# Performance work log

Measured on AMD Instinct MI355X. Metric: run time of the kernel, lower is better.

Reference implementation:

```python
import jax, jax.numpy as jnp
import numpy as np

B, V, D, NH, DH = 1, 6, 256, 8, 32
L, ZP = 4, 4
BEV = 80
Q = BEV * BEV
SHAPES = [(56, 100), (28, 50), (14, 25), (7, 13)]
N = sum(h * w for h, w in SHAPES)
PAD_H, PAD_W = 448, 800
PC = (-48.0, -48.0, -5.0, 48.0, 48.0, 3.0)
EPS = 1e-5


def _ref3d():
    # get_reference_points + pc_range scaling; the original overwrites the z channel
    # with scaled-x (code bug: ref_3d[...,2:3] = ref_3d[...,:1]*zrange+zmin) -> reproduced faithfully,
    # so all ZP pillar points are identical.
    u = jnp.arange(Q)
    xs = ((u % BEV).astype(jnp.float32) + 0.5) / BEV
    ys = ((u // BEV).astype(jnp.float32) + 0.5) / BEV
    x = xs * (PC[3] - PC[0]) + PC[0]
    y = ys * (PC[4] - PC[1]) + PC[1]
    z = x * (PC[5] - PC[2]) + PC[2]
    p = jnp.stack([x, y, z], -1)  # [Q,3]
    return jnp.broadcast_to(p[None], (ZP, Q, 3))


def _project(l2i):
    # l2i: [B,V,4,4] -> normalized coords [B,V,Q,ZP,2], validity mask [B,V,Q,ZP]
    pts = _ref3d().reshape(-1, 3)
    pts_h = jnp.concatenate([pts, jnp.ones_like(pts[:, :1])], -1)  # [ZP*Q,4]
    ip = jnp.einsum('bvij,nj->bvni', l2i, pts_h)                   # [B,V,ZP*Q,4]
    zc = ip[..., 2]
    xy = ip[..., :2] / jnp.clip(zc, EPS, None)[..., None]
    xn = xy[..., 0] / PAD_W
    yn = xy[..., 1] / PAD_H
    m = (zc > EPS) & (xn > 0) & (xn < 1) & (yn > 0) & (yn < 1)
    coords = jnp.stack([xn, yn], -1).reshape(B, V, ZP, Q, 2).transpose(0, 1, 3, 2, 4)
    mask = m.reshape(B, V, ZP, Q).transpose(0, 1, 3, 2)
    return coords, mask


def _forward(feat0, feat1, feat2, feat3, lidar2img_mat, bev_emb, level_embeds,
             view_embeds, value_W, value_b, off_W, off_b, aw_W, aw_b, out_W, out_b):
    feats = [feat0, feat1, feat2, feat3]
    parts = []
    for l, f in enumerate(feats):
        h, w = SHAPES[l]
        x = f.reshape(B, V, D, h * w).transpose(0, 1, 3, 2)  # [B,V,hw,D]
        x = x + view_embeds[None, :, None, :] + level_embeds[l]
        parts.append(x)
    feat_flat = jnp.concatenate(parts, axis=2)  # [B,V,N,D]

    coords, mask = _project(lidar2img_mat)
    mask_any = mask.any(-1)                                            # [B,V,Q]
    count = jnp.clip(mask_any.sum(1).astype(jnp.float32), 1.0, None)   # [B,Q]

    value = (feat_flat.reshape(B * V, N, D) @ value_W + value_b).reshape(B * V, N, NH, DH)
    off = (bev_emb @ off_W + off_b).reshape(Q, NH, L, ZP, 2)
    aw = jax.nn.softmax((bev_emb @ aw_W + aw_b).reshape(Q, NH, L * ZP), -1).reshape(Q, NH, L, ZP)
    ref = coords.reshape(B * V, Q, ZP, 2)

    out = jnp.zeros((B * V, Q, NH, DH), feat_flat.dtype)
    start = 0
    for l, (h, w) in enumerate(SHAPES):
        v_l = value[:, start:start + h * w].transpose(0, 2, 1, 3).reshape(B * V * NH, h * w, DH)
        start += h * w
        loc = ref[:, :, None, :, :] + off[None, :, :, l] / jnp.array([w, h], feat_flat.dtype)
        loc = loc.transpose(0, 2, 1, 3, 4).reshape(B * V * NH, Q * ZP, 2)
        # grid_sample(align_corners=False, padding='zeros') with grid 2*loc-1
        gx = loc[..., 0] * w - 0.5
        gy = loc[..., 1] * h - 0.5
        x0 = jnp.floor(gx).astype(jnp.int32)
        y0 = jnp.floor(gy).astype(jnp.int32)
        wx1 = gx - x0
        wy1 = gy - y0

        def corner(xi, yi, wt):
            valid = (xi >= 0) & (xi < w) & (yi >= 0) & (yi < h)
            lin = jnp.clip(yi, 0, h - 1) * w + jnp.clip(xi, 0, w - 1)
            g = jnp.take_along_axis(v_l, lin[..., None], axis=1)
            return g * (wt * valid)[..., None]

        s = (corner(x0, y0, (1 - wx1) * (1 - wy1)) + corner(x0 + 1, y0, wx1 * (1 - wy1))
             + corner(x0, y0 + 1, (1 - wx1) * wy1) + corner(x0 + 1, y0 + 1, wx1 * wy1))
        s = s.reshape(B * V, NH, Q, ZP, DH)
        out = out + jnp.einsum('vhqzd,qhz->vqhd', s, aw[:, :, l])

    attn = out.reshape(B, V, Q, D)
    slots = (attn * mask_any[..., None]).sum(1) / count[..., None]
    slots = slots @ out_W + out_b
    return bev_emb[None] + slots  # dropout is identity at inference


def setup_inputs() -> dict:
    key = jax.random.key(0)
    ks = jax.random.split(key, 16)
    s = 0.02
    return {
        'feat0': jax.random.normal(ks[0], (B, V, D) + SHAPES[0], jnp.float32),
        'feat1': jax.random.normal(ks[1], (B, V, D) + SHAPES[1], jnp.float32),
        'feat2': jax.random.normal(ks[2], (B, V, D) + SHAPES[2], jnp.float32),
        'feat3': jax.random.normal(ks[3], (B, V, D) + SHAPES[3], jnp.float32),
        'lidar2img_mat': jax.random.normal(ks[4], (B, V, 4, 4), jnp.float32) * 50.0,
        'bev_emb': jax.random.normal(ks[5], (Q, D), jnp.float32) * s,
        'level_embeds': jax.random.normal(ks[6], (L, D), jnp.float32) * s,
        'view_embeds': jax.random.normal(ks[7], (V, D), jnp.float32) * s,
        'value_W': jax.random.normal(ks[8], (D, D), jnp.float32) * s,
        'value_b': jnp.zeros((D,), jnp.float32),
        'off_W': jax.random.normal(ks[9], (D, NH * L * ZP * 2), jnp.float32) * s,
        'off_b': jnp.zeros((NH * L * ZP * 2,), jnp.float32),
        'aw_W': jax.random.normal(ks[10], (D, NH * L * ZP), jnp.float32) * s,
        'aw_b': jnp.zeros((NH * L * ZP,), jnp.float32),
        'out_W': jax.random.normal(ks[11], (D, D), jnp.float32) * s,
        'out_b': jnp.zeros((D,), jnp.float32),
    }


def reference(feat0, feat1, feat2, feat3, lidar2img_mat, bev_emb, level_embeds,
              view_embeds, value_W, value_b, off_W, off_b, aw_W, aw_b, out_W, out_b):
    return _forward(feat0, feat1, feat2, feat3, lidar2img_mat, bev_emb, level_embeds,
                    view_embeds, value_W, value_b, off_W, off_b, aw_W, aw_b, out_W, out_b)
```

## Files before the change

### kernel.cpp

```cpp
#include <hip/hip_runtime.h>
#include <cstdint>
#include <cstddef>

#define NV 6
#define ND 256
#define NHEAD 8
#define NBEV 80
#define NQ 6400
#define NTOK 7441
#define MROWS (NV * NTOK)
#define FEPS 1e-5f

#define VROWT 698
#define VBLKS (VROWT * 2)
#define OABLKS 300
#define GBLKS (VBLKS + OABLKS)
#define GCHUNK (GBLKS / 8)

typedef __attribute__((ext_vector_type(8))) short bfx8;
typedef __attribute__((ext_vector_type(4))) float fx4;
typedef __attribute__((ext_vector_type(4))) _Float16 hx4;
typedef __attribute__((ext_vector_type(4))) unsigned short usx4;

__device__ __forceinline__ unsigned short f2bf(float x) {
    uint32_t u = __builtin_bit_cast(uint32_t, x);
    u += 0x7FFFu + ((u >> 16) & 1u);
    return (unsigned short)(u >> 16);
}
__device__ __forceinline__ float lof(uint32_t u) {
    return __builtin_bit_cast(float, u << 16);
}
__device__ __forceinline__ float hif(uint32_t u) {
    return __builtin_bit_cast(float, u & 0xFFFF0000u);
}

__global__ __launch_bounds__(256) void k_prep(
        const float* __restrict__ l2i, const float* __restrict__ ve,
        const float* __restrict__ le, const float* __restrict__ vW,
        const float* __restrict__ vB, const float* __restrict__ oW,
        const float* __restrict__ aW, const float* __restrict__ outW,
        float2* __restrict__ coords, int* __restrict__ mask,
        unsigned short* __restrict__ vWt, unsigned short* __restrict__ oaWt,
        unsigned short* __restrict__ outWt, float* __restrict__ emb_proj) {
    int bid = blockIdx.x;
    int t = threadIdx.x;
    if (bid < 150) {
        int idx = bid * 256 + t;
        int v = idx / NQ, q = idx - v * NQ;
        float xs = ((float)(q % NBEV) + 0.5f) / (float)NBEV;
        float ys = ((float)(q / NBEV) + 0.5f) / (float)NBEV;
        float x = xs * 96.0f - 48.0f;
        float y = ys * 96.0f - 48.0f;
        float z = x * 8.0f - 5.0f;
        const float* M = l2i + v * 16;
        float ip0 = M[0] * x + M[1] * y + M[2] * z + M[3];
        float ip1 = M[4] * x + M[5] * y + M[6] * z + M[7];
        float ip2 = M[8] * x + M[9] * y + M[10] * z + M[11];
        float dz = fmaxf(ip2, FEPS);
        float xn = ip0 / dz / 800.0f;
        float yn = ip1 / dz / 448.0f;
        bool m = (ip2 > FEPS) && (xn > 0.0f) && (xn < 1.0f) && (yn > 0.0f) && (yn < 1.0f);
        coords[idx] = make_float2(xn, yn);
        mask[idx] = m ? 1 : 0;
    } else if (bid < 406) {
        int e = (bid - 150) * 256 + t;
        int k = e >> 8, n = e & 255;
        vWt[(size_t)n * 256 + k] = f2bf(vW[(size_t)k * 256 + n]);
    } else if (bid < 662) {
        int e = (bid - 406) * 256 + t;
        int k = e >> 8, n = e & 255;
        oaWt[(size_t)n * 256 + k] = f2bf(oW[(size_t)k * 256 + n]);
    } else if (bid < 790) {
        int e = (bid - 662) * 256 + t;
        int k = e >> 7, n = e & 127;
        oaWt[(size_t)(256 + n) * 256 + k] = f2bf(aW[(size_t)k * 128 + n]);
    } else if (bid < 1046) {
        int e = (bid - 790) * 256 + t;
        int k = e >> 8, n = e & 255;
        outWt[(size_t)n * 256 + k] = f2bf(outW[(size_t)k * 256 + n]);
    } else {
        int blk = bid - 1046;
        int v = blk >> 2, l = blk & 3;
        float acc = vB[t];
        for (int d = 0; d < ND; ++d)
            acc += (ve[v * ND + d] + le[l * ND + d]) * vW[d * ND + t];
        emb_proj[blk * ND + t] = acc;
    }
}

__global__ __launch_bounds__(256) void k_gemms(
        const float* __restrict__ f0, const float* __restrict__ f1,
        const float* __restrict__ f2, const float* __restrict__ f3,
        const unsigned short* __restrict__ vWt, const float* __restrict__ emb_proj,
        unsigned short* __restrict__ value,
        const float* __restrict__ bev, const unsigned short* __restrict__ oaWt,
        const float* __restrict__ oB, const float* __restrict__ aB,
        float* __restrict__ off, float* __restrict__ aw_pre) {
    __shared__ unsigned short As[64][40];
    __shared__ unsigned short Bs[128][40];
    __shared__ const float* rowptr[64];
    __shared__ int rowstride[64];
    __shared__ int rowemb[64];
    int b = blockIdx.x;
    int lb = (b & 7) * GCHUNK + (b >> 3);
    int t = threadIdx.x;
    int lane = t & 63, w = t >> 6;
    int wm = w >> 1, wn = w & 1;
    int lr = lane & 15, lk = lane >> 4;
    int mA = t & 63, kg = t >> 6;

    fx4 acc[2][4];
#pragma unroll
    for (int i = 0; i < 2; ++i)
#pragma unroll
        for (int j = 0; j < 4; ++j) acc[i][j] = (fx4)0.0f;

    if (lb < VBLKS) {
        int m0 = (lb >> 1) * 64, c0 = (lb & 1) * 128;
        if (t < 64) {
            int m = m0 + t;
            if (m >= MROWS) m = MROWS - 1;
            int v = m / NTOK, n = m - v * NTOK;
            int l, p, hw;
            const float* base;
            if (n < 5600)      { l = 0; p = n;        hw = 5600; base = f0; }
            else if (n < 7000) { l = 1; p = n - 5600; hw = 1400; base = f1; }
            else if (n < 7350) { l = 2; p = n - 7000; hw = 350;  base = f2; }
            else               { l = 3; p = n - 7350; hw = 91;   base = f3; }
            rowptr[t] = base + (size_t)v * ND * hw + p;
            rowstride[t] = hw;
            rowemb[t] = v * 4 + l;
        }
        __syncthreads();
        const unsigned short* bp = vWt + (size_t)(c0 + (t >> 1)) * 256 + (t & 1) * 16;
        const float* rp = rowptr[mA];
        int rs = rowstride[mA];
        for (int k0 = 0; k0 < 256; k0 += 32) {
            float va[8];
#pragma unroll
            for (int i = 0; i < 8; ++i)
                va[i] = rp[(size_t)(k0 + kg * 8 + i) * rs];
            bfx8 a8;
#pragma unroll
            for (int i = 0; i < 8; ++i) a8[i] = (short)f2bf(va[i]);
            *(bfx8*)&As[mA][kg * 8] = a8;
            *(bfx8*)&Bs[t >> 1][(t & 1) * 16] = *(const bfx8*)(bp + k0);
            *(bfx8*)&Bs[t >> 1][(t & 1) * 16 + 8] = *(const bfx8*)(bp + k0 + 8);
            __syncthreads();
            bfx8 af[2], bf[4];
#pragma unroll
            for (int f = 0; f < 2; ++f)
                af[f] = *(bfx8*)&As[wm * 32 + f * 16 + lr][lk * 8];
#pragma unroll
            for (int f = 0; f < 4; ++f)
                bf[f] = *(bfx8*)&Bs[wn * 64 + f * 16 + lr][lk * 8];
#pragma unroll
            for (int fm = 0; fm < 2; ++fm)
#pragma unroll
                for (int fn = 0; fn < 4; ++fn)
                    acc[fm][fn] = __builtin_amdgcn_mfma_f32_16x16x32_bf16(
                        af[fm], bf[fn], acc[fm][fn], 0, 0, 0);
            __syncthreads();
        }
#pragma unroll
        for (int fm = 0; fm < 2; ++fm) {
#pragma unroll
            for (int fn = 0; fn < 4; ++fn) {
                int col = c0 + wn * 64 + fn * 16 + lr;
#pragma unroll
                for (int r = 0; r < 4; ++r) {
                    int rl = wm * 32 + fm * 16 + lk * 4 + r;
                    int m = m0 + rl;
                    if (m < MROWS) {
                        float e = emb_proj[(size_t)rowemb[rl] * ND + col];
                        value[(size_t)m * ND + col] = f2bf(acc[fm][fn][r] + e);
                    }
                }
            }
        }
    } else {
        int r6 = lb - VBLKS;
        int m0 = (r6 / 3) * 64, c0 = (r6 % 3) * 128;
        const float* ap = bev + (size_t)(m0 + mA) * 256 + kg * 8;
        const unsigned short* bp = oaWt + (size_t)(c0 + (t >> 1)) * 256 + (t & 1) * 16;
        for (int k0 = 0; k0 < 256; k0 += 32) {
            float va[8];
            *(float4*)&va[0] = *(const float4*)(ap + k0);
            *(float4*)&va[4] = *(const float4*)(ap + k0 + 4);
            bfx8 a8;
#pragma unroll
            for (int i = 0; i < 8; ++i) a8[i] = (short)f2bf(va[i]);
            *(bfx8*)&As[mA][kg * 8] = a8;
            *(bfx8*)&Bs[t >> 1][(t & 1) * 16] = *(const bfx8*)(bp + k0);
            *(bfx8*)&Bs[t >> 1][(t & 1) * 16 + 8] = *(const bfx8*)(bp + k0 + 8);
            __syncthreads();
            bfx8 af[2], bf[4];
#pragma unroll
            for (int f = 0; f < 2; ++f)
                af[f] = *(bfx8*)&As[wm * 32 + f * 16 + lr][lk * 8];
#pragma unroll
            for (int f = 0; f < 4; ++f)
                bf[f] = *(bfx8*)&Bs[wn * 64 + f * 16 + lr][lk * 8];
#pragma unroll
            for (int fm = 0; fm < 2; ++fm)
#pragma unroll
                for (int fn = 0; fn < 4; ++fn)
                    acc[fm][fn] = __builtin_amdgcn_mfma_f32_16x16x32_bf16(
                        af[fm], bf[fn], acc[fm][fn], 0, 0, 0);
            __syncthreads();
        }
        if (c0 < 256) {
#pragma unroll
            for (int fm = 0; fm < 2; ++fm) {
#pragma unroll
                for (int fn = 0; fn < 4; ++fn) {
                    int col = c0 + wn * 64 + fn * 16 + lr;
                    float bs = oB[col];
#pragma unroll
                    for (int r = 0; r < 4; ++r) {
                        int m = m0 + wm * 32 + fm * 16 + lk * 4 + r;
                        off[(size_t)m * 256 + col] = acc[fm][fn][r] + bs;
                    }
                }
            }
        } else {
#pragma unroll
            for (int fm = 0; fm < 2; ++fm) {
#pragma unroll
                for (int fn = 0; fn < 4; ++fn) {
                    int col = wn * 64 + fn * 16 + lr;
                    float bs = aB[col];
#pragma unroll
                    for (int r = 0; r < 4; ++r) {
                        int m = m0 + wm * 32 + fm * 16 + lk * 4 + r;
                        aw_pre[(size_t)m * 128 + col] = acc[fm][fn][r] + bs;
                    }
                }
            }
        }
    }
}

#define SQB 2
__global__ __launch_bounds__(256) void k_sample(
        const float2* __restrict__ coords, const int* __restrict__ mask,
        const float* __restrict__ off, const float* __restrict__ awlog,
        const unsigned short* __restrict__ value, float* __restrict__ slots) {
    __shared__ float aw_s[SQB][128];
    __shared__ unsigned short lin_s[SQB][NV][128][4];
    __shared__ _Float16 w_s[SQB][NV][128][4];
    __shared__ float2 cxy_s[SQB][NV];
    __shared__ int msk_s[SQB][NV];

    int b = blockIdx.x;
    int lb = (b & 7) * (NQ / SQB / 8) + (b >> 3);
    int q0 = lb * SQB;
    int t = threadIdx.x;
    if (t < SQB * NV) {
        int qq = t / NV, v = t - qq * NV;
        msk_s[qq][v] = mask[v * NQ + q0 + qq];
        cxy_s[qq][v] = coords[v * NQ + q0 + qq];
    }
    {
        int qq = t >> 7, c2 = t & 127;
        aw_s[qq][c2] = awlog[(size_t)(q0 + qq) * 128 + c2];
    }
    __syncthreads();
    if (t < SQB * NHEAD) {
        int qq = t >> 3, h = t & 7;
        float* p = &aw_s[qq][h * 16];
        float mx = p[0];
#pragma unroll
        for (int i = 1; i < 16; ++i) mx = fmaxf(mx, p[i]);
        float e[16];
        float s = 0.0f;
#pragma unroll
        for (int i = 0; i < 16; ++i) { e[i] = __expf(p[i] - mx); s += e[i]; }
        float inv = 1.0f / s;
#pragma unroll
        for (int i = 0; i < 16; ++i) p[i] = e[i] * inv;
    }
    __syncthreads();

    const int LW[4] = {100, 50, 25, 13};
    const int LH[4] = {56, 28, 14, 7};
    const int LST[4] = {0, 5600, 7000, 7350};
    for (int idx = t; idx < SQB * NV * 128; idx += 256) {
        int c2 = idx & 127;
        int rem = idx >> 7;
        int qq = rem / NV, v = rem - qq * NV;
        if (!msk_s[qq][v]) continue;
        int ll = (c2 >> 2) & 3;
        int iwl = LW[ll], ihl = LH[ll], st = LST[ll];
        float wl = (float)iwl, hl = (float)ihl;
        float2 o2 = *(const float2*)&off[(size_t)(q0 + qq) * 256 + 2 * c2];
        float2 cc = cxy_s[qq][v];
        float gx = cc.x * wl + o2.x - 0.5f;
        float gy = cc.y * hl + o2.y - 0.5f;
        float fxf = floorf(gx), fyf = floorf(gy);
        int x0 = (int)fxf, y0 = (int)fyf;
        float wx = gx - fxf, wy = gy - fyf;
        bool bx0 = (unsigned)x0 < (unsigned)iwl;
        bool bx1 = (unsigned)(x0 + 1) < (unsigned)iwl;
        bool by0 = (unsigned)y0 < (unsigned)ihl;
        bool by1 = (unsigned)(y0 + 1) < (unsigned)ihl;
        int cx0 = min(max(x0, 0), iwl - 1);
        int cx1 = min(max(x0 + 1, 0), iwl - 1);
        int cy0 = min(max(y0, 0), ihl - 1);
        int cy1 = min(max(y0 + 1, 0), ihl - 1);
        float wa = aw_s[qq][c2];
        int r0 = st + cy0 * iwl, r1 = st + cy1 * iwl;
        usx4 lin;
        lin.x = (unsigned short)(r0 + cx0);
        lin.y = (unsigned short)(r0 + cx1);
        lin.z = (unsigned short)(r1 + cx0);
        lin.w = (unsigned short)(r1 + cx1);
        hx4 ww;
        ww.x = (_Float16)((bx0 && by0) ? (1.0f - wx) * (1.0f - wy) * wa : 0.0f);
        ww.y = (_Float16)((bx1 && by0) ? wx * (1.0f - wy) * wa : 0.0f);
        ww.z = (_Float16)((bx0 && by1) ? (1.0f - wx) * wy * wa : 0.0f);
        ww.w = (_Float16)((bx1 && by1) ? wx * wy * wa : 0.0f);
        *(usx4*)lin_s[qq][v][c2] = lin;
        *(hx4*)w_s[qq][v][c2] = ww;
    }
    __syncthreads();

    int qq = t >> 7, cp = t & 127;
    int hb = (cp >> 4) * 16;
    float acc0 = 0.0f, acc1 = 0.0f;
    int cnt = 0;
#pragma unroll
    for (int v = 0; v < NV; ++v) cnt += msk_s[qq][v];
    for (int v = 0; v < NV; ++v) {
        if (!msk_s[qq][v]) continue;
        const uint32_t* vb = (const uint32_t*)(value + (size_t)v * NTOK * 256) + cp;
#pragma unroll
        for (int ci = 0; ci < 16; ++ci) {
            int c2 = hb + ci;
            usx4 lin = *(const usx4*)lin_s[qq][v][c2];
            hx4 wh = *(const hx4*)w_s[qq][v][c2];
            uint32_t u0 = vb[(size_t)lin.x * 128];
            uint32_t u1 = vb[(size_t)lin.y * 128];
            uint32_t u2 = vb[(size_t)lin.z * 128];
            uint32_t u3 = vb[(size_t)lin.w * 128];
            float w0 = (float)wh.x, w1 = (float)wh.y;
            float w2 = (float)wh.z, w3 = (float)wh.w;
            acc0 += w0 * lof(u0) + w1 * lof(u1) + w2 * lof(u2) + w3 * lof(u3);
            acc1 += w0 * hif(u0) + w1 * hif(u1) + w2 * hif(u2) + w3 * hif(u3);
        }
    }
    float invc = 1.0f / fmaxf((float)cnt, 1.0f);
    *(float2*)&slots[(size_t)(q0 + qq) * 256 + 2 * cp] = make_float2(acc0 * invc, acc1 * invc);
}

__global__ __launch_bounds__(256) void k_out(
        const float* __restrict__ A, const unsigned short* __restrict__ Bt,
        const float* __restrict__ bias, const float* __restrict__ addsrc,
        float* __restrict__ out) {
    __shared__ unsigned short As[64][40];
    __shared__ unsigned short Bs[128][40];
    int t = threadIdx.x;
    int m0 = blockIdx.x * 64, c0 = blockIdx.y * 128;
    int lane = t & 63, w = t >> 6;
    int wm = w >> 1, wn = w & 1;
    int lr = lane & 15, lk = lane >> 4;
    int mA = t & 63, kg = t >> 6;
    const float* ap = A + (size_t)(m0 + mA) * 256 + kg * 8;
    const unsigned short* bp = Bt + (size_t)(c0 + (t >> 1)) * 256 + (t & 1) * 16;
    fx4 acc[2][4];
#pragma unroll
    for (int i = 0; i < 2; ++i)
#pragma unroll
        for (int j = 0; j < 4; ++j) acc[i][j] = (fx4)0.0f;
    for (int k0 = 0; k0 < 256; k0 += 32) {
        float va[8];
        *(float4*)&va[0] = *(const float4*)(ap + k0);
        *(float4*)&va[4] = *(const float4*)(ap + k0 + 4);
        bfx8 a8;
#pragma unroll
        for (int i = 0; i < 8; ++i) a8[i] = (short)f2bf(va[i]);
        *(bfx8*)&As[mA][kg * 8] = a8;
        *(bfx8*)&Bs[t >> 1][(t & 1) * 16] = *(const bfx8*)(bp + k0);
        *(bfx8*)&Bs[t >> 1][(t & 1) * 16 + 8] = *(const bfx8*)(bp + k0 + 8);
        __syncthreads();
        bfx8 af[2], bf[4];
#pragma unroll
        for (int f = 0; f < 2; ++f)
            af[f] = *(bfx8*)&As[wm * 32 + f * 16 + lr][lk * 8];
#pragma unroll
        for (int f = 0; f < 4; ++f)
            bf[f] = *(bfx8*)&Bs[wn * 64 + f * 16 + lr][lk * 8];
#pragma unroll
        for (int fm = 0; fm < 2; ++fm)
#pragma unroll
            for (int fn = 0; fn < 4; ++fn)
                acc[fm][fn] = __builtin_amdgcn_mfma_f32_16x16x32_bf16(
                    af[fm], bf[fn], acc[fm][fn], 0, 0, 0);
        __syncthreads();
    }
#pragma unroll
    for (int fm = 0; fm < 2; ++fm) {
#pragma unroll
        for (int fn = 0; fn < 4; ++fn) {
            int col = c0 + wn * 64 + fn * 16 + lr;
            float bs = bias[col];
#pragma unroll
            for (int r = 0; r < 4; ++r) {
                int m = m0 + wm * 32 + fm * 16 + lk * 4 + r;
                out[(size_t)m * 256 + col] =
                    acc[fm][fn][r] + bs + addsrc[(size_t)m * 256 + col];
            }
        }
    }
}

extern "C" void kernel_launch(void* const* d_in, const int* in_sizes, int n_in,
                              void* d_out, int out_size, void* d_ws, size_t ws_size,
                              hipStream_t stream) {
    const float* f0   = (const float*)d_in[0];
    const float* f1   = (const float*)d_in[1];
    const float* f2   = (const float*)d_in[2];
    const float* f3   = (const float*)d_in[3];
    const float* l2i  = (const float*)d_in[4];
    const float* bev  = (const float*)d_in[5];
    const float* le   = (const float*)d_in[6];
    const float* ve   = (const float*)d_in[7];
    const float* vW   = (const float*)d_in[8];
    const float* vB   = (const float*)d_in[9];
    const float* oW   = (const float*)d_in[10];
    const float* oB   = (const float*)d_in[11];
    const float* aW   = (const float*)d_in[12];
    const float* aB   = (const float*)d_in[13];
    const float* outW = (const float*)d_in[14];
    const float* outB = (const float*)d_in[15];
    float* out = (float*)d_out;

    char* ws = (char*)d_ws;
    size_t o = 0;
    auto alloc = [&](size_t bytes) {
        void* p = ws + o;
        o += (bytes + 255) & ~(size_t)255;
        return p;
    };
    float2* coords   = (float2*)alloc((size_t)NV * NQ * sizeof(float2));
    int*    mask     = (int*)alloc((size_t)NV * NQ * sizeof(int));
    float*  emb_proj = (float*)alloc((size_t)24 * ND * sizeof(float));
    float*  off      = (float*)alloc((size_t)NQ * 256 * sizeof(float));
    float*  aw_pre   = (float*)alloc((size_t)NQ * 128 * sizeof(float));
    float*  slots    = (float*)alloc((size_t)NQ * 256 * sizeof(float));
    unsigned short* value = (unsigned short*)alloc((size_t)MROWS * ND * sizeof(short));
    unsigned short* vWt   = (unsigned short*)alloc((size_t)256 * 256 * sizeof(short));
    unsigned short* oaWt  = (unsigned short*)alloc((size_t)384 * 256 * sizeof(short));
    unsigned short* outWt = (unsigned short*)alloc((size_t)256 * 256 * sizeof(short));

    k_prep<<<1070, 256, 0, stream>>>(l2i, ve, le, vW, vB, oW, aW, outW,
                                     coords, mask, vWt, oaWt, outWt, emb_proj);
    k_gemms<<<GBLKS, 256, 0, stream>>>(f0, f1, f2, f3, vWt, emb_proj, value,
                                       bev, oaWt, oB, aB, off, aw_pre);
    k_sample<<<NQ / SQB, 256, 0, stream>>>(coords, mask, off, aw_pre, value, slots);
    dim3 gout(NQ / 64, 2);
    k_out<<<gout, 256, 0, stream>>>(slots, outWt, outB, bev, out);
}
```

Before: 204.6 us.

## Pre-transpose features to bf16 row-major and enlarge GEMM tiles to 128x128

The prep kernel now transposes the channel-major feature maps into a token-major bf16 buffer through a shared-memory tile, and converts the BEV embedding to bf16. The GEMM kernel can then load A with contiguous vector reads instead of strided fp32 gathers. It also moves to 128x128 tiles with a 64-wide K step, giving more MFMA work per block. The cost is an extra round trip of the transposed data through global memory and fewer, larger GEMM blocks.

```diff
diff --git a/kernel.cpp b/kernel.cpp
--- a/kernel.cpp
+++ b/kernel.cpp
@@ -9,13 +9,24 @@
 #define NQ 6400
 #define NTOK 7441
 #define MROWS (NV * NTOK)
+#define MROWSP 44672
 #define FEPS 1e-5f
 
-#define VROWT 698
-#define VBLKS (VROWT * 2)
-#define OABLKS 300
-#define GBLKS (VBLKS + OABLKS)
+#define VBLKS 698
+#define GBLKS 848
 #define GCHUNK (GBLKS / 8)
+
+#define PR_PROJ 150
+#define PR_TR   2832
+#define PR_BEV  800
+#define PB0 PR_PROJ
+#define PB1 (PB0 + PR_TR)
+#define PB2 (PB1 + PR_BEV)
+#define PB3 (PB2 + 256)
+#define PB4 (PB3 + 256)
+#define PB5 (PB4 + 128)
+#define PB6 (PB5 + 256)
+#define PBT (PB6 + 24)
 
 typedef __attribute__((ext_vector_type(8))) short bfx8;
 typedef __attribute__((ext_vector_type(4))) float fx4;
@@ -35,16 +46,20 @@
 }
 
 __global__ __launch_bounds__(256) void k_prep(
-        const float* __restrict__ l2i, const float* __restrict__ ve,
-        const float* __restrict__ le, const float* __restrict__ vW,
-        const float* __restrict__ vB, const float* __restrict__ oW,
-        const float* __restrict__ aW, const float* __restrict__ outW,
+        const float* __restrict__ f0, const float* __restrict__ f1,
+        const float* __restrict__ f2, const float* __restrict__ f3,
+        const float* __restrict__ l2i, const float* __restrict__ bev,
+        const float* __restrict__ ve, const float* __restrict__ le,
+        const float* __restrict__ vW, const float* __restrict__ vB,
+        const float* __restrict__ oW, const float* __restrict__ aW,
+        const float* __restrict__ outW,
         float2* __restrict__ coords, int* __restrict__ mask,
+        unsigned short* __restrict__ featT, unsigned short* __restrict__ bevh,
         unsigned short* __restrict__ vWt, unsigned short* __restrict__ oaWt,
         unsigned short* __restrict__ outWt, float* __restrict__ emb_proj) {
     int bid = blockIdx.x;
     int t = threadIdx.x;
-    if (bid < 150) {
+    if (bid < PB0) {
         int idx = bid * 256 + t;
         int v = idx / NQ, q = idx - v * NQ;
         float xs = ((float)(q % NBEV) + 0.5f) / (float)NBEV;
@@ -62,24 +77,63 @@
         bool m = (ip2 > FEPS) && (xn > 0.0f) && (xn < 1.0f) && (yn > 0.0f) && (yn < 1.0f);
         coords[idx] = make_float2(xn, yn);
         mask[idx] = m ? 1 : 0;
-    } else if (bid < 406) {
-        int e = (bid - 150) * 256 + t;
+    } else if (bid < PB1) {
+        __shared__ float T[64][65];
+        int idx = bid - PB0;
+        int v = idx / 472;
+        int rem = idx - v * 472;
+        int mt = rem >> 2, kt = rem & 3;
+        int hw, p0, st;
+        const float* base;
+        if (mt < 88)       { base = f0; hw = 5600; st = 0;    p0 = mt * 64; }
+        else if (mt < 110) { base = f1; hw = 1400; st = 5600; p0 = (mt - 88) * 64; }
+        else if (mt < 116) { base = f2; hw = 350;  st = 7000; p0 = (mt - 110) * 64; }
+        else               { base = f3; hw = 91;   st = 7350; p0 = (mt - 116) * 64; }
+        int k0 = kt * 64;
+        const float* src = base + (size_t)v * 256 * hw;
+#pragma unroll
+        for (int i = 0; i < 16; ++i) {
+            int ii = t + i * 256;
+            int kk = ii >> 6, mm = ii & 63;
+            float val = (p0 + mm < hw) ? src[(size_t)(k0 + kk) * hw + p0 + mm] : 0.0f;
+            T[kk][mm] = val;
+        }
+        __syncthreads();
+#pragma unroll
+        for (int i = 0; i < 16; ++i) {
+            int ii = t + i * 256;
+            int mm = ii >> 6, kk = ii & 63;
+            if (p0 + mm < hw)
+                featT[(size_t)(v * NTOK + st + p0 + mm) * 256 + k0 + kk] = f2bf(T[kk][mm]);
+        }
+    } else if (bid < PB2) {
+        size_t e = (size_t)(bid - PB1) * 2048 + t * 8;
+        float4 a = *(const float4*)(bev + e);
+        float4 b = *(const float4*)(bev + e + 4);
+        bfx8 o;
+        o[0] = (short)f2bf(a.x); o[1] = (short)f2bf(a.y);
+        o[2] = (short)f2bf(a.z); o[3] = (short)f2bf(a.w);
+        o[4] = (short)f2bf(b.x); o[5] = (short)f2bf(b.y);
+        o[6] = (short)f2bf(b.z); o[7] = (short)f2bf(b.w);
+        *(bfx8*)(bevh + e) = o;
+    } else if (bid < PB3) {
+        int e = (bid - PB2) * 256 + t;
         int k = e >> 8, n = e & 255;
         vWt[(size_t)n * 256 + k] = f2bf(vW[(size_t)k * 256 + n]);
-    } else if (bid < 662) {
-        int e = (bid - 406) * 256 + t;
+    } else if (bid < PB4) {
+        int e = (bid - PB3) * 256 + t;
         int k = e >> 8, n = e & 255;
         oaWt[(size_t)n * 256 + k] = f2bf(oW[(size_t)k * 256 + n]);
-    } else if (bid < 790) {
-        int e = (bid - 662) * 256 + t;
+    } else if (bid < PB5) {
+        int e = (bid - PB4) * 256 + t;
         int k = e >> 7, n = e & 127;
         oaWt[(size_t)(256 + n) * 256 + k] = f2bf(aW[(size_t)k * 128 + n]);
-    } else if (bid < 1046) {
-        int e = (bid - 790) * 256 + t;
+    } else if (bid < PB6) {
+        int e = (bid - PB5) * 256 + t;
         int k = e >> 8, n = e & 255;
         outWt[(size_t)n * 256 + k] = f2bf(outW[(size_t)k * 256 + n]);
     } else {
-        int blk = bid - 1046;
+        int blk = bid - PB6;
         int v = blk >> 2, l = blk & 3;
         float acc = vB[t];
         for (int d = 0; d < ND; ++d)
@@ -89,152 +143,122 @@
 }
 
 __global__ __launch_bounds__(256) void k_gemms(
-        const float* __restrict__ f0, const float* __restrict__ f1,
-        const float* __restrict__ f2, const float* __restrict__ f3,
+        const unsigned short* __restrict__ featT,
         const unsigned short* __restrict__ vWt, const float* __restrict__ emb_proj,
         unsigned short* __restrict__ value,
-        const float* __restrict__ bev, const unsigned short* __restrict__ oaWt,
+        const unsigned short* __restrict__ bevh,
+        const unsigned short* __restrict__ oaWt,
         const float* __restrict__ oB, const float* __restrict__ aB,
         float* __restrict__ off, float* __restrict__ aw_pre) {
-    __shared__ unsigned short As[64][40];
-    __shared__ unsigned short Bs[128][40];
-    __shared__ const float* rowptr[64];
-    __shared__ int rowstride[64];
-    __shared__ int rowemb[64];
+    __shared__ unsigned short As[128][72];
+    __shared__ unsigned short Bs[128][72];
     int b = blockIdx.x;
     int lb = (b & 7) * GCHUNK + (b >> 3);
     int t = threadIdx.x;
     int lane = t & 63, w = t >> 6;
     int wm = w >> 1, wn = w & 1;
     int lr = lane & 15, lk = lane >> 4;
-    int mA = t & 63, kg = t >> 6;
-
-    fx4 acc[2][4];
-#pragma unroll
-    for (int i = 0; i < 2; ++i)
+
+    bool isval = lb < VBLKS;
+    int m0, c0;
+    const unsigned short *ap, *bp;
+    if (isval) {
+        m0 = (lb >> 1) * 128; c0 = (lb & 1) * 128;
+        ap = featT; bp = vWt;
+    } else {
+        int r6 = lb - VBLKS;
+        m0 = (r6 / 3) * 128; c0 = (r6 % 3) * 128;
+        ap = bevh; bp = oaWt;
+    }
+    int sr = t >> 1, sk = (t & 1) * 32;
+    const unsigned short* arow = ap + (size_t)(m0 + sr) * 256 + sk;
+    const unsigned short* brow = bp + (size_t)(c0 + sr) * 256 + sk;
+
+    fx4 acc[4][4];
+#pragma unroll
+    for (int i = 0; i < 4; ++i)
 #pragma unroll
         for (int j = 0; j < 4; ++j) acc[i][j] = (fx4)0.0f;
 
-    if (lb < VBLKS) {
-        int m0 = (lb >> 1) * 64, c0 = (lb & 1) * 128;
-        if (t < 64) {
-            int m = m0 + t;
-            if (m >= MROWS) m = MROWS - 1;
-            int v = m / NTOK, n = m - v * NTOK;
-            int l, p, hw;
-            const float* base;
-            if (n < 5600)      { l = 0; p = n;        hw = 5600; base = f0; }
-            else if (n < 7000) { l = 1; p = n - 5600; hw = 1400; base = f1; }
-            else if (n < 7350) { l = 2; p = n - 7000; hw = 350;  base = f2; }
-            else               { l = 3; p = n - 7350; hw = 91;   base = f3; }
-            rowptr[t] = base + (size_t)v * ND * hw + p;
-            rowstride[t] = hw;
-            rowemb[t] = v * 4 + l;
-        }
+    for (int k0 = 0; k0 < 256; k0 += 64) {
+        bfx8 a0 = *(const bfx8*)(arow + k0);
+        bfx8 a1 = *(const bfx8*)(arow + k0 + 8);
+        bfx8 a2 = *(const bfx8*)(arow + k0 + 16);
+        bfx8 a3 = *(const bfx8*)(arow + k0 + 24);
+        bfx8 b0 = *(const bfx8*)(brow + k0);
+        bfx8 b1 = *(const bfx8*)(brow + k0 + 8);
+        bfx8 b2 = *(const bfx8*)(brow + k0 + 16);
+        bfx8 b3 = *(const bfx8*)(brow + k0 + 24);
+        *(bfx8*)&As[sr][sk]      = a0;
+        *(bfx8*)&As[sr][sk + 8]  = a1;
+        *(bfx8*)&As[sr][sk + 16] = a2;
+        *(bfx8*)&As[sr][sk + 24] = a3;
+        *(bfx8*)&Bs[sr][sk]      = b0;
+        *(bfx8*)&Bs[sr][sk + 8]  = b1;
+        *(bfx8*)&Bs[sr][sk + 16] = b2;
+        *(bfx8*)&Bs[sr][sk + 24] = b3;
         __syncthreads();
-        const unsigned short* bp = vWt + (size_t)(c0 + (t >> 1)) * 256 + (t & 1) * 16;
-        const float* rp = rowptr[mA];
-        int rs = rowstride[mA];
-        for (int k0 = 0; k0 < 256; k0 += 32) {
-            float va[8];
-#pragma unroll
-            for (int i = 0; i < 8; ++i)
-                va[i] = rp[(size_t)(k0 + kg * 8 + i) * rs];
-            bfx8 a8;
-#pragma unroll
-            for (int i = 0; i < 8; ++i) a8[i] = (short)f2bf(va[i]);
-            *(bfx8*)&As[mA][kg * 8] = a8;
-            *(bfx8*)&Bs[t >> 1][(t & 1) * 16] = *(const bfx8*)(bp + k0);
-            *(bfx8*)&Bs[t >> 1][(t & 1) * 16 + 8] = *(const bfx8*)(bp + k0 + 8);
-            __syncthreads();
-            bfx8 af[2], bf[4];
-#pragma unroll
-            for (int f = 0; f < 2; ++f)
-                af[f] = *(bfx8*)&As[wm * 32 + f * 16 + lr][lk * 8];
-#pragma unroll
-            for (int f = 0; f < 4; ++f)
-                bf[f] = *(bfx8*)&Bs[wn * 64 + f * 16 + lr][lk * 8];
-#pragma unroll
-            for (int fm = 0; fm < 2; ++fm)
+#pragma unroll
+        for (int ks = 0; ks < 64; ks += 32) {
+            bfx8 af[4], bf[4];
+#pragma unroll
+            for (int f = 0; f < 4; ++f) {
+                af[f] = *(bfx8*)&As[wm * 64 + f * 16 + lr][ks + lk * 8];
+                bf[f] = *(bfx8*)&Bs[wn * 64 + f * 16 + lr][ks + lk * 8];
+            }
+#pragma unroll
+            for (int fm = 0; fm < 4; ++fm)
 #pragma unroll
                 for (int fn = 0; fn < 4; ++fn)
                     acc[fm][fn] = __builtin_amdgcn_mfma_f32_16x16x32_bf16(
                         af[fm], bf[fn], acc[fm][fn], 0, 0, 0);
-            __syncthreads();
-        }
-#pragma unroll
-        for (int fm = 0; fm < 2; ++fm) {
+        }
+        __syncthreads();
+    }
+
+    if (isval) {
+#pragma unroll
+        for (int fm = 0; fm < 4; ++fm) {
+#pragma unroll
+            for (int r = 0; r < 4; ++r) {
+                int m = m0 + wm * 64 + fm * 16 + lk * 4 + r;
+                if (m >= MROWS) continue;
+                int v = m / NTOK;
+                int n = m - v * NTOK;
+                int l = (n < 5600) ? 0 : (n < 7000) ? 1 : (n < 7350) ? 2 : 3;
+                const float* ep = emb_proj + (size_t)(v * 4 + l) * ND;
+#pragma unroll
+                for (int fn = 0; fn < 4; ++fn) {
+                    int col = c0 + wn * 64 + fn * 16 + lr;
+                    value[(size_t)m * ND + col] = f2bf(acc[fm][fn][r] + ep[col]);
+                }
+            }
+        }
+    } else if (c0 < 256) {
+#pragma unroll
+        for (int fm = 0; fm < 4; ++fm) {
 #pragma unroll
             for (int fn = 0; fn < 4; ++fn) {
                 int col = c0 + wn * 64 + fn * 16 + lr;
+                float bs = oB[col];
 #pragma unroll
                 for (int r = 0; r < 4; ++r) {
-                    int rl = wm * 32 + fm * 16 + lk * 4 + r;
-                    int m = m0 + rl;
-                    if (m < MROWS) {
-                        float e = emb_proj[(size_t)rowemb[rl] * ND + col];
-                        value[(size_t)m * ND + col] = f2bf(acc[fm][fn][r] + e);
-                    }
+                    int m = m0 + wm * 64 + fm * 16 + lk * 4 + r;
+                    off[(size_t)m * 256 + col] = acc[fm][fn][r] + bs;
                 }
             }
         }
     } else {
-        int r6 = lb - VBLKS;
-        int m0 = (r6 / 3) * 64, c0 = (r6 % 3) * 128;
-        const float* ap = bev + (size_t)(m0 + mA) * 256 + kg * 8;
-        const unsigned short* bp = oaWt + (size_t)(c0 + (t >> 1)) * 256 + (t & 1) * 16;
-        for (int k0 = 0; k0 < 256; k0 += 32) {
-            float va[8];
-            *(float4*)&va[0] = *(const float4*)(ap + k0);
-            *(float4*)&va[4] = *(const float4*)(ap + k0 + 4);
-            bfx8 a8;
-#pragma unroll
-            for (int i = 0; i < 8; ++i) a8[i] = (short)f2bf(va[i]);
-            *(bfx8*)&As[mA][kg * 8] = a8;
-            *(bfx8*)&Bs[t >> 1][(t & 1) * 16] = *(const bfx8*)(bp + k0);
-            *(bfx8*)&Bs[t >> 1][(t & 1) * 16 + 8] = *(const bfx8*)(bp + k0 + 8);
-            __syncthreads();
-            bfx8 af[2], bf[4];
-#pragma unroll
-            for (int f = 0; f < 2; ++f)
-                af[f] = *(bfx8*)&As[wm * 32 + f * 16 + lr][lk * 8];
-#pragma unroll
-            for (int f = 0; f < 4; ++f)
-                bf[f] = *(bfx8*)&Bs[wn * 64 + f * 16 + lr][lk * 8];
-#pragma unroll
-            for (int fm = 0; fm < 2; ++fm)
-#pragma unroll
-                for (int fn = 0; fn < 4; ++fn)
-                    acc[fm][fn] = __builtin_amdgcn_mfma_f32_16x16x32_bf16(
-                        af[fm], bf[fn], acc[fm][fn], 0, 0, 0);
-            __syncthreads();
-        }
-        if (c0 < 256) {
-#pragma unroll
-            for (int fm = 0; fm < 2; ++fm) {
-#pragma unroll
-                for (int fn = 0; fn < 4; ++fn) {
-                    int col = c0 + wn * 64 + fn * 16 + lr;
-                    float bs = oB[col];
-#pragma unroll
-                    for (int r = 0; r < 4; ++r) {
-                        int m = m0 + wm * 32 + fm * 16 + lk * 4 + r;
-                        off[(size_t)m * 256 + col] = acc[fm][fn][r] + bs;
-                    }
-                }
-            }
-        } else {
-#pragma unroll
-            for (int fm = 0; fm < 2; ++fm) {
-#pragma unroll
-                for (int fn = 0; fn < 4; ++fn) {
-                    int col = wn * 64 + fn * 16 + lr;
-                    float bs = aB[col];
-#pragma unroll
-                    for (int r = 0; r < 4; ++r) {
-                        int m = m0 + wm * 32 + fm * 16 + lk * 4 + r;
-                        aw_pre[(size_t)m * 128 + col] = acc[fm][fn][r] + bs;
-                    }
+#pragma unroll
+        for (int fm = 0; fm < 4; ++fm) {
+#pragma unroll
+            for (int fn = 0; fn < 4; ++fn) {
+                int col = wn * 64 + fn * 16 + lr;
+                float bs = aB[col];
+#pragma unroll
+                for (int r = 0; r < 4; ++r) {
+                    int m = m0 + wm * 64 + fm * 16 + lk * 4 + r;
+                    aw_pre[(size_t)m * 128 + col] = acc[fm][fn][r] + bs;
                 }
             }
         }
@@ -449,14 +473,17 @@
     float*  aw_pre   = (float*)alloc((size_t)NQ * 128 * sizeof(float));
     float*  slots    = (float*)alloc((size_t)NQ * 256 * sizeof(float));
     unsigned short* value = (unsigned short*)alloc((size_t)MROWS * ND * sizeof(short));
+    unsigned short* featT = (unsigned short*)alloc((size_t)MROWSP * ND * sizeof(short));
+    unsigned short* bevh  = (unsigned short*)alloc((size_t)NQ * ND * sizeof(short));
     unsigned short* vWt   = (unsigned short*)alloc((size_t)256 * 256 * sizeof(short));
     unsigned short* oaWt  = (unsigned short*)alloc((size_t)384 * 256 * sizeof(short));
     unsigned short* outWt = (unsigned short*)alloc((size_t)256 * 256 * sizeof(short));
 
-    k_prep<<<1070, 256, 0, stream>>>(l2i, ve, le, vW, vB, oW, aW, outW,
-                                     coords, mask, vWt, oaWt, outWt, emb_proj);
-    k_gemms<<<GBLKS, 256, 0, stream>>>(f0, f1, f2, f3, vWt, emb_proj, value,
-                                       bev, oaWt, oB, aB, off, aw_pre);
+    k_prep<<<PBT, 256, 0, stream>>>(f0, f1, f2, f3, l2i, bev, ve, le, vW, vB,
+                                    oW, aW, outW, coords, mask, featT, bevh,
+                                    vWt, oaWt, outWt, emb_proj);
+    k_gemms<<<GBLKS, 256, 0, stream>>>(featT, vWt, emb_proj, value,
+                                       bevh, oaWt, oB, aB, off, aw_pre);
     k_sample<<<NQ / SQB, 256, 0, stream>>>(coords, mask, off, aw_pre, value, slots);
     dim3 gout(NQ / 64, 2);
     k_out<<<gout, 256, 0, stream>>>(slots, outWt, outB, bev, out);
```

Result: faster. 186.7 us (-8.7%).
